# Optimization experiments

Measured on AMD Instinct MI355X. Metric: run time of the kernel, lower is better.

Reference implementation:

```python
import jax, jax.numpy as jnp
import numpy as np

B, S, D, H = 2, 2048, 1024, 16
DQ = D // H
EPS = 1e-5


def setup_inputs() -> dict:
    key = jax.random.key(0)
    ks = jax.random.split(key, 6)
    scale = 0.02
    return {
        "x": jax.random.normal(ks[0], (B, S, D), dtype=jnp.float32),
        "ln_g": jnp.ones((D,), dtype=jnp.float32),
        "ln_b": jnp.zeros((D,), dtype=jnp.float32),
        "Wq": jax.random.normal(ks[1], (D, D), dtype=jnp.float32) * scale,
        "bq": jnp.zeros((D,), dtype=jnp.float32),
        "Wk": jax.random.normal(ks[2], (D, D), dtype=jnp.float32) * scale,
        "bk": jnp.zeros((D,), dtype=jnp.float32),
        "Wv": jax.random.normal(ks[3], (D, D), dtype=jnp.float32) * scale,
        "bv": jnp.zeros((D,), dtype=jnp.float32),
        "Wo": jax.random.normal(ks[4], (D, D), dtype=jnp.float32) * scale,
        "bo": jnp.zeros((D,), dtype=jnp.float32),
    }


def reference(x, ln_g, ln_b, Wq, bq, Wk, bk, Wv, bv, Wo, bo):
    # pre-LayerNorm (torch default eps=1e-5, biased variance)
    mu = jnp.mean(x, axis=-1, keepdims=True)
    var = jnp.mean((x - mu) ** 2, axis=-1, keepdims=True)
    xn = (x - mu) * jax.lax.rsqrt(var + EPS) * ln_g + ln_b

    # QKV projections; weights stored [d_in, d_out]
    q = xn @ Wq + bq  # [B,S,D]
    k = xn @ Wk + bk
    v = xn @ Wv + bv

    # split heads -> [B,H,S,DQ]
    def heads(t):
        return t.reshape(B, S, H, DQ).transpose(0, 2, 1, 3)
    q, k, v = heads(q), heads(k), heads(v)

    scores = jnp.einsum("bhqd,bhkd->bhqk", q, k) / jnp.sqrt(jnp.float32(DQ))
    causal = jnp.tril(jnp.ones((S, S), dtype=bool))  # True = keep
    scores = jnp.where(causal, scores, -jnp.inf)
    probs = jax.nn.softmax(scores, axis=-1)
    attn = jnp.einsum("bhqk,bhkd->bhqd", probs, v)  # [B,H,S,DQ]

    # merge heads: [B,H,S,DQ] -> [B,S,H*DQ] (matches transpose/flatten/transpose)
    merged = attn.transpose(0, 2, 1, 3).reshape(B, S, D)
    out = merged @ Wo + bo
    return out + x
```

## Files before the change

### kernel.cpp

```cpp
#include <hip/hip_runtime.h>
#include <math.h>

#define BB 2
#define SS 2048
#define DD 1024
#define HH 16
#define DQK 64
#define NROWS (BB * SS)
#define NE ((size_t)BB * SS * DD)

using short8 = __attribute__((ext_vector_type(8))) short;
using f32x4  = __attribute__((ext_vector_type(4))) float;

__device__ __forceinline__ ushort f2bf(float f) {
  union { float f; unsigned u; } c; c.f = f;
  return (ushort)((c.u + 0x7fffu + ((c.u >> 16) & 1u)) >> 16);
}

__device__ __forceinline__ unsigned cvt_pk_bf16(float lo, float hi) {
  unsigned r;
  asm("v_cvt_pk_bf16_f32 %0, %1, %2" : "=v"(r) : "v"(lo), "v"(hi));
  return r;
}

__device__ __forceinline__ f32x4 mfma16(short8 a, short8 b, f32x4 c) {
  return __builtin_amdgcn_mfma_f32_16x16x32_bf16(a, b, c, 0, 0, 0);
}

typedef __attribute__((address_space(1))) const unsigned gas_u32;
typedef __attribute__((address_space(3))) unsigned las_u32;
__device__ __forceinline__ void gload_lds16(const void* g, void* l) {
  __builtin_amdgcn_global_load_lds((gas_u32*)g, (las_u32*)l, 16, 0, 0);
}

__global__ __launch_bounds__(256) void prep(const float* __restrict__ x,
                                            const float* __restrict__ g,
                                            const float* __restrict__ bta,
                                            ushort* __restrict__ xn,
                                            const float* __restrict__ Wq,
                                            const float* __restrict__ Wk,
                                            const float* __restrict__ Wv,
                                            const float* __restrict__ Wo,
                                            ushort* __restrict__ wt) {
  __shared__ float tile[64][65];
  const int t = threadIdx.x;
  if (blockIdx.x < NROWS) {
    const int row = blockIdx.x;
    float4 v = ((const float4*)(x + (size_t)row * DD))[t];
    float s  = v.x + v.y + v.z + v.w;
    float ss = v.x * v.x + v.y * v.y + v.z * v.z + v.w * v.w;
#pragma unroll
    for (int off = 32; off > 0; off >>= 1) {
      s  += __shfl_xor(s, off);
      ss += __shfl_xor(ss, off);
    }
    const int wid = t >> 6, lane = t & 63;
    if (lane == 0) { tile[0][wid] = s; tile[0][4 + wid] = ss; }
    __syncthreads();
    const float stot  = tile[0][0] + tile[0][1] + tile[0][2] + tile[0][3];
    const float sstot = tile[0][4] + tile[0][5] + tile[0][6] + tile[0][7];
    const float mu  = stot * (1.0f / DD);
    const float var = sstot * (1.0f / DD) - mu * mu;
    const float inv = rsqrtf(var + 1e-5f);
    const float4 g4 = ((const float4*)g)[t];
    const float4 b4 = ((const float4*)bta)[t];
    ushort4 o;
    o.x = f2bf((v.x - mu) * inv * g4.x + b4.x);
    o.y = f2bf((v.y - mu) * inv * g4.y + b4.y);
    o.z = f2bf((v.z - mu) * inv * g4.z + b4.z);
    o.w = f2bf((v.w - mu) * inv * g4.w + b4.w);
    ((ushort4*)(xn + (size_t)row * DD))[t] = o;
  } else {
    const int wb = blockIdx.x - NROWS;
    const int z = wb >> 8;
    const int k0 = (wb & 15) * 64, n0 = ((wb >> 4) & 15) * 64;
    const float* W = (z == 0) ? Wq : (z == 1) ? Wk : (z == 2) ? Wv : Wo;
    ushort* dst = wt + (size_t)z * DD * DD;
    const int tr = t >> 4, tc = (t & 15) * 4;
#pragma unroll
    for (int rr = 0; rr < 64; rr += 16) {
      float4 v = *(const float4*)(W + (size_t)(k0 + rr + tr) * DD + n0 + tc);
      tile[rr + tr][tc + 0] = v.x;
      tile[rr + tr][tc + 1] = v.y;
      tile[rr + tr][tc + 2] = v.z;
      tile[rr + tr][tc + 3] = v.w;
    }
    __syncthreads();
#pragma unroll
    for (int rr = 0; rr < 64; rr += 16) {
      const int n = rr + tr;
      ushort4 o;
      o.x = f2bf(tile[tc + 0][n]);
      o.y = f2bf(tile[tc + 1][n]);
      o.z = f2bf(tile[tc + 2][n]);
      o.w = f2bf(tile[tc + 3][n]);
      *(ushort4*)(dst + (size_t)(n0 + n) * DD + k0 + tc) = o;
    }
  }
}

#define GEMM_CORE(Ag, Bg)                                                     \
  f32x4 acc[4][4];                                                            \
  _Pragma("unroll")                                                           \
  for (int m = 0; m < 4; ++m)                                                 \
    _Pragma("unroll")                                                         \
    for (int n = 0; n < 4; ++n) acc[m][n] = (f32x4){0.f, 0.f, 0.f, 0.f};     \
  const int cs = ((t & 3) * 16) ^ (((t >> 2) & 3) * 16);                      \
  const int fsw = (r16 & 3) * 16;                                             \
  {                                                                           \
    GSTAGE(Ag, Bg, 0, 0);                                                     \
    int cur = 0;                                                              \
    for (int k0 = 0; k0 < DD; k0 += 32) {                                     \
      asm volatile("s_waitcnt vmcnt(0)" ::: "memory");                        \
      __syncthreads();                                                        \
      if (k0 + 32 < DD) GSTAGE(Ag, Bg, cur ^ 1, k0 + 32);                     \
      const char* Ac = (const char*)&As[cur][0][0];                           \
      const char* Bc = (const char*)&Bs[cur][0][0];                           \
      short8 af[4], bf[4];                                                    \
      _Pragma("unroll")                                                       \
      for (int m = 0; m < 4; ++m)                                             \
        af[m] = *(const short8*)(Ac + (wr * 64 + m * 16 + r16) * 64 +         \
                                 ((g * 16) ^ fsw));                           \
      _Pragma("unroll")                                                       \
      for (int n = 0; n < 4; ++n)                                             \
        bf[n] = *(const short8*)(Bc + (wc * 64 + n * 16 + r16) * 64 +         \
                                 ((g * 16) ^ fsw));                           \
      _Pragma("unroll")                                                       \
      for (int m = 0; m < 4; ++m)                                             \
        _Pragma("unroll")                                                     \
        for (int n = 0; n < 4; ++n) acc[m][n] = mfma16(af[m], bf[n], acc[m][n]); \
      cur ^= 1;                                                               \
    }                                                                         \
  }

#define GSTAGE(Ag, Bg, buf, k0)                                               \
  {                                                                           \
    _Pragma("unroll")                                                         \
    for (int i = 0; i < 2; ++i) {                                             \
      gload_lds16(Ag + (size_t)(row0 + i * 64 + (t >> 2)) * (DD * 2) +        \
                      (k0) * 2 + cs,                                          \
                  (char*)&As[buf][0][0] + i * 4096 + t * 16);                 \
      gload_lds16(Bg + (size_t)(col0 + i * 64 + (t >> 2)) * (DD * 2) +        \
                      (k0) * 2 + cs,                                          \
                  (char*)&Bs[buf][0][0] + i * 4096 + t * 16);                 \
    }                                                                         \
  }

__global__ __launch_bounds__(256) void gemm_qkv(
    const ushort* __restrict__ A, const ushort* __restrict__ wt,
    const float* __restrict__ bq, const float* __restrict__ bk,
    const float* __restrict__ bv, ushort* __restrict__ qb,
    ushort* __restrict__ kb, ushort* __restrict__ vt) {
  __shared__ ushort As[2][128][32];
  __shared__ ushort Bs[2][128][32];
  const int t = threadIdx.x;
  const int lane = t & 63;
  const int w = t >> 6, wr = w >> 1, wc = w & 1;
  const int r16 = lane & 15, g = lane >> 4;
  const int row0 = blockIdx.x * 128;
  const int mat = blockIdx.y >> 3;
  const int col0 = (blockIdx.y & 7) * 128;
  const char* Ag = (const char*)A;
  const char* Bg = (const char*)(wt + (size_t)mat * DD * DD);
  const float* bias = (mat == 0) ? bq : (mat == 1) ? bk : bv;
  const float scl = (mat == 0) ? 0.125f * 1.44269504f : 1.0f;

  GEMM_CORE(Ag, Bg)

#pragma unroll
  for (int n = 0; n < 4; ++n) {
    const int c = col0 + wc * 64 + n * 16 + r16;
    const float bc = bias[c];
#pragma unroll
    for (int m = 0; m < 4; ++m) {
      const int rbase = row0 + wr * 64 + m * 16 + g * 4;
      if (mat < 2) {
        ushort* outb = (mat == 0) ? qb : kb;
#pragma unroll
        for (int e = 0; e < 4; ++e)
          outb[(size_t)(rbase + e) * DD + c] = f2bf((acc[m][n][e] + bc) * scl);
      } else {
        uint2 st;
        st.x = cvt_pk_bf16(acc[m][n][0] + bc, acc[m][n][1] + bc);
        st.y = cvt_pk_bf16(acc[m][n][2] + bc, acc[m][n][3] + bc);
        const size_t vrow = (size_t)((rbase >> 11) * HH + (c >> 6)) * DQK + (c & 63);
        *(uint2*)(vt + vrow * SS + (rbase & 2047)) = st;
      }
    }
  }
}

__global__ __launch_bounds__(256) void gemm_o(
    const ushort* __restrict__ A, const ushort* __restrict__ Bt,
    const float* __restrict__ bias, const float* __restrict__ resid,
    float* __restrict__ outf) {
  __shared__ ushort As[2][128][32];
  __shared__ ushort Bs[2][128][32];
  const int t = threadIdx.x;
  const int lane = t & 63;
  const int w = t >> 6, wr = w >> 1, wc = w & 1;
  const int r16 = lane & 15, g = lane >> 4;
  const int row0 = blockIdx.x * 128;
  const int col0 = blockIdx.y * 128;
  const char* Ag = (const char*)A;
  const char* Bg = (const char*)Bt;

  GEMM_CORE(Ag, Bg)

#pragma unroll
  for (int n = 0; n < 4; ++n) {
    const int c = col0 + wc * 64 + n * 16 + r16;
    const float bc = bias[c];
#pragma unroll
    for (int m = 0; m < 4; ++m) {
      const int rbase = row0 + wr * 64 + m * 16 + g * 4;
#pragma unroll
      for (int e = 0; e < 4; ++e) {
        const size_t idx = (size_t)(rbase + e) * DD + c;
        outf[idx] = acc[m][n][e] + bc + resid[idx];
      }
    }
  }
}

__global__ __launch_bounds__(256) void attn_mfma(const ushort* __restrict__ Q,
                                                 const ushort* __restrict__ K,
                                                 const ushort* __restrict__ Vt,
                                                 ushort* __restrict__ O) {
  __shared__ ushort Ks[2][64][64];
  __shared__ ushort Vs[2][64][64];

  const int t = threadIdx.x, lane = t & 63, ww = t >> 6;
  const int r16 = lane & 15, g = lane >> 4;

  const int bid = blockIdx.x;
  const int xcd = bid & 7;
  const int bh = xcd * 4 + ((bid >> 3) & 3);
  const int m = (bid >> 5) & 7;
  const int j = bid >> 8;
  const int qb = (j == 0) ? (31 - m) : (j == 1) ? m : (j == 2) ? (23 - m) : (8 + m);
  const int b = bh >> 4, h = bh & 15;
  const size_t tokbase = (size_t)b * SS;
  const size_t hoff = (size_t)h * DQK;
  const int q0 = qb * 64 + ww * 16;
  const int nt = qb + 1;

  const int srow = t >> 3;
  const int scol = (t & 7) * 16;
  const char* Kb = (const char*)(K + tokbase * DD + hoff);
  const char* Vb = (const char*)(Vt + (size_t)bh * DQK * SS);
  const int sw = (r16 & 7) << 4;
  const int rlo = (r16 & 3) + ((r16 >> 2) << 3);

#define STAGE(buf, j0)                                                        \
  {                                                                           \
    _Pragma("unroll")                                                         \
    for (int i = 0; i < 2; ++i) {                                             \
      const int R = i * 32 + srow;                                            \
      const int Cs = scol ^ ((R & 7) << 4);                                   \
      gload_lds16(Kb + ((size_t)((j0) + R) * DD) * 2 + Cs,                    \
                  (char*)&Ks[buf][0][0] + i * 4096 + ww * 1024);              \
      gload_lds16(Vb + ((size_t)R * SS + (j0)) * 2 + Cs,                      \
                  (char*)&Vs[buf][0][0] + i * 4096 + ww * 1024);              \
    }                                                                         \
  }

  short8 qf[2];
#pragma unroll
  for (int kc = 0; kc < 2; ++kc)
    qf[kc] = *(const short8*)(Q + (tokbase + q0 + r16) * DD + hoff + kc * 32 + g * 8);

  f32x4 o[4];
#pragma unroll
  for (int dt = 0; dt < 4; ++dt) o[dt] = (f32x4){0.f, 0.f, 0.f, 0.f};
  float rm = -INFINITY, rl = 0.f;

  STAGE(0, 0);
  int cur = 0;
  for (int tt = 0; tt < nt; ++tt) {
    asm volatile("s_waitcnt vmcnt(0)" ::: "memory");
    __syncthreads();
    if (tt + 1 < nt) STAGE(cur ^ 1, (tt + 1) * 64);

    const char* Kc = (const char*)&Ks[cur][0][0];
    const char* Vc = (const char*)&Vs[cur][0][0];

    f32x4 s4[4];
    __builtin_amdgcn_s_setprio(1);
#pragma unroll
    for (int t2 = 0; t2 < 4; ++t2) {
      const int kk = rlo + (t2 & 1) * 4 + (t2 >> 1) * 32;
      const int sk = (kk & 7) << 4;
      const int rb = kk * 128;
      const short8 k0 = *(const short8*)(Kc + rb + ((g * 16) ^ sk));
      const short8 k1 = *(const short8*)(Kc + rb + ((64 + g * 16) ^ sk));
      f32x4 s = mfma16(k0, qf[0], (f32x4){0.f, 0.f, 0.f, 0.f});
      s4[t2] = mfma16(k1, qf[1], s);
    }
    __builtin_amdgcn_s_setprio(0);

    if (tt == nt - 1) {
      const int thrl = q0 + r16 - g * 8 - tt * 64;
#pragma unroll
      for (int t2 = 0; t2 < 4; ++t2) {
        const int bb = (t2 & 1) * 4 + (t2 >> 1) * 32;
#pragma unroll
        for (int r = 0; r < 4; ++r)
          s4[t2][r] = (bb + r <= thrl) ? s4[t2][r] : -INFINITY;
      }
    }

    float mx = fmaxf(
        fmaxf(fmaxf(fmaxf(s4[0][0], s4[0][1]), fmaxf(s4[0][2], s4[0][3])),
              fmaxf(fmaxf(s4[1][0], s4[1][1]), fmaxf(s4[1][2], s4[1][3]))),
        fmaxf(fmaxf(fmaxf(s4[2][0], s4[2][1]), fmaxf(s4[2][2], s4[2][3])),
              fmaxf(fmaxf(s4[3][0], s4[3][1]), fmaxf(s4[3][2], s4[3][3]))));

    if (!__all(mx - rm <= 8.f)) {
      float mf = fmaxf(mx, __shfl_xor(mx, 16));
      mf = fmaxf(mf, __shfl_xor(mf, 32));
      const float mn = fmaxf(rm, mf);
      const float sc = __builtin_amdgcn_exp2f(rm - mn);
      rl *= sc;
#pragma unroll
      for (int dt = 0; dt < 4; ++dt) o[dt] *= sc;
      rm = mn;
    }

    union { unsigned u[4]; short8 s; } pbu[2];
#pragma unroll
    for (int t2 = 0; t2 < 4; ++t2) {
      const float p0 = __builtin_amdgcn_exp2f(s4[t2][0] - rm);
      const float p1 = __builtin_amdgcn_exp2f(s4[t2][1] - rm);
      const float p2 = __builtin_amdgcn_exp2f(s4[t2][2] - rm);
      const float p3 = __builtin_amdgcn_exp2f(s4[t2][3] - rm);
      rl += (p0 + p1) + (p2 + p3);
      pbu[t2 >> 1].u[(t2 & 1) * 2 + 0] = cvt_pk_bf16(p0, p1);
      pbu[t2 >> 1].u[(t2 & 1) * 2 + 1] = cvt_pk_bf16(p2, p3);
    }

    __builtin_amdgcn_s_setprio(1);
#pragma unroll
    for (int kc = 0; kc < 2; ++kc) {
#pragma unroll
      for (int dt = 0; dt < 4; ++dt) {
        const short8 vf = *(const short8*)(Vc + (dt * 16 + r16) * 128 +
                                           ((kc * 64 + g * 16) ^ sw));
        o[dt] = mfma16(vf, pbu[kc].s, o[dt]);
      }
    }
    __builtin_amdgcn_s_setprio(0);
    cur ^= 1;
  }
#undef STAGE

  rl += __shfl_xor(rl, 16);
  rl += __shfl_xor(rl, 32);
  const float inv = 1.0f / rl;
#pragma unroll
  for (int dt = 0; dt < 4; ++dt) {
    uint2 st;
    st.x = cvt_pk_bf16(o[dt][0] * inv, o[dt][1] * inv);
    st.y = cvt_pk_bf16(o[dt][2] * inv, o[dt][3] * inv);
    *(uint2*)(O + (tokbase + q0 + r16) * DD + hoff + dt * 16 + g * 4) = st;
  }
}

extern "C" void kernel_launch(void* const* d_in, const int* in_sizes, int n_in,
                              void* d_out, int out_size, void* d_ws, size_t ws_size,
                              hipStream_t stream) {
  const float* x    = (const float*)d_in[0];
  const float* ln_g = (const float*)d_in[1];
  const float* ln_b = (const float*)d_in[2];
  const float* Wq   = (const float*)d_in[3];
  const float* bq   = (const float*)d_in[4];
  const float* Wk   = (const float*)d_in[5];
  const float* bk   = (const float*)d_in[6];
  const float* Wv   = (const float*)d_in[7];
  const float* bv   = (const float*)d_in[8];
  const float* Wo   = (const float*)d_in[9];
  const float* bo   = (const float*)d_in[10];
  float* out = (float*)d_out;

  ushort* ws  = (ushort*)d_ws;
  ushort* xn  = ws;
  ushort* qb  = xn + NE;
  ushort* kb  = qb + NE;
  ushort* vt  = kb + NE;
  ushort* ab  = vt + NE;
  ushort* wt  = ab + NE;
  ushort* wot = wt + (size_t)3 * DD * DD;

  prep<<<NROWS + 1024, 256, 0, stream>>>(x, ln_g, ln_b, xn, Wq, Wk, Wv, Wo, wt);

  gemm_qkv<<<dim3(NROWS / 128, 24), 256, 0, stream>>>(xn, wt, bq, bk, bv,
                                                      qb, kb, vt);

  attn_mfma<<<BB * HH * (SS / 64), 256, 0, stream>>>(qb, kb, vt, ab);

  gemm_o<<<dim3(NROWS / 128, DD / 128), 256, 0, stream>>>(ab, wot, bo, x, out);
}
```

Before: 115.0 us.

## Triple-buffer GEMM LDS staging and retune LDS swizzles in GEMM and attention

The GEMM main loop goes from double to triple buffering. It prefetches two k-steps ahead and waits with vmcnt(4) instead of draining all loads each iteration, to hide more global-load latency. The LDS XOR swizzle patterns in both the GEMM and attention kernels change, likely to reduce bank conflicts on ds_read. Plain __syncthreads is replaced by s_barrier wrapped in sched_barrier fences to control instruction scheduling. The cost is 50% more LDS per GEMM block, which could lower occupancy, and the vmcnt(4) count must match the number of loads GSTAGE issues.

```diff
diff --git a/kernel.cpp b/kernel.cpp
--- a/kernel.cpp
+++ b/kernel.cpp
@@ -105,17 +105,27 @@
   for (int m = 0; m < 4; ++m)                                                 \
     _Pragma("unroll")                                                         \
     for (int n = 0; n < 4; ++n) acc[m][n] = (f32x4){0.f, 0.f, 0.f, 0.f};     \
-  const int cs = ((t & 3) * 16) ^ (((t >> 2) & 3) * 16);                      \
-  const int fsw = (r16 & 3) * 16;                                             \
+  const int cs = ((t & 3) * 16) ^ (((t >> 3) & 3) * 16);                      \
+  const int fsw = ((r16 >> 1) & 3) * 16;                                      \
   {                                                                           \
     GSTAGE(Ag, Bg, 0, 0);                                                     \
-    int cur = 0;                                                              \
+    GSTAGE(Ag, Bg, 1, 32);                                                    \
+    int cb = 0;                                                               \
     for (int k0 = 0; k0 < DD; k0 += 32) {                                     \
-      asm volatile("s_waitcnt vmcnt(0)" ::: "memory");                        \
-      __syncthreads();                                                        \
-      if (k0 + 32 < DD) GSTAGE(Ag, Bg, cur ^ 1, k0 + 32);                     \
-      const char* Ac = (const char*)&As[cur][0][0];                           \
-      const char* Bc = (const char*)&Bs[cur][0][0];                           \
+      __builtin_amdgcn_sched_barrier(0);                                      \
+      if (k0 + 32 < DD) {                                                     \
+        asm volatile("s_waitcnt vmcnt(4)" ::: "memory");                      \
+      } else {                                                                \
+        asm volatile("s_waitcnt vmcnt(0)" ::: "memory");                      \
+      }                                                                       \
+      __builtin_amdgcn_s_barrier();                                           \
+      __builtin_amdgcn_sched_barrier(0);                                      \
+      if (k0 + 64 < DD) {                                                     \
+        int nb = cb + 2; if (nb >= 3) nb -= 3;                                \
+        GSTAGE(Ag, Bg, nb, k0 + 64);                                          \
+      }                                                                       \
+      const char* Ac = (const char*)&As[cb][0][0];                            \
+      const char* Bc = (const char*)&Bs[cb][0][0];                            \
       short8 af[4], bf[4];                                                    \
       _Pragma("unroll")                                                       \
       for (int m = 0; m < 4; ++m)                                             \
@@ -129,7 +139,7 @@
       for (int m = 0; m < 4; ++m)                                             \
         _Pragma("unroll")                                                     \
         for (int n = 0; n < 4; ++n) acc[m][n] = mfma16(af[m], bf[n], acc[m][n]); \
-      cur ^= 1;                                                               \
+      cb = (cb + 1 == 3) ? 0 : cb + 1;                                        \
     }                                                                         \
   }
 
@@ -151,8 +161,8 @@
     const float* __restrict__ bq, const float* __restrict__ bk,
     const float* __restrict__ bv, ushort* __restrict__ qb,
     ushort* __restrict__ kb, ushort* __restrict__ vt) {
-  __shared__ ushort As[2][128][32];
-  __shared__ ushort Bs[2][128][32];
+  __shared__ ushort As[3][128][32];
+  __shared__ ushort Bs[3][128][32];
   const int t = threadIdx.x;
   const int lane = t & 63;
   const int w = t >> 6, wr = w >> 1, wc = w & 1;
@@ -194,8 +204,8 @@
     const ushort* __restrict__ A, const ushort* __restrict__ Bt,
     const float* __restrict__ bias, const float* __restrict__ resid,
     float* __restrict__ outf) {
-  __shared__ ushort As[2][128][32];
-  __shared__ ushort Bs[2][128][32];
+  __shared__ ushort As[3][128][32];
+  __shared__ ushort Bs[3][128][32];
   const int t = threadIdx.x;
   const int lane = t & 63;
   const int w = t >> 6, wr = w >> 1, wc = w & 1;
@@ -249,7 +259,7 @@
   const int scol = (t & 7) * 16;
   const char* Kb = (const char*)(K + tokbase * DD + hoff);
   const char* Vb = (const char*)(Vt + (size_t)bh * DQK * SS);
-  const int sw = (r16 & 7) << 4;
+  const int sw = ((r16 & 3) | ((r16 >> 1) & 4)) << 4;
   const int rlo = (r16 & 3) + ((r16 >> 2) << 3);
 
 #define STAGE(buf, j0)                                                        \
@@ -257,7 +267,7 @@
     _Pragma("unroll")                                                         \
     for (int i = 0; i < 2; ++i) {                                             \
       const int R = i * 32 + srow;                                            \
-      const int Cs = scol ^ ((R & 7) << 4);                                   \
+      const int Cs = scol ^ (((R & 3) | ((R >> 1) & 4)) << 4);                \
       gload_lds16(Kb + ((size_t)((j0) + R) * DD) * 2 + Cs,                    \
                   (char*)&Ks[buf][0][0] + i * 4096 + ww * 1024);              \
       gload_lds16(Vb + ((size_t)R * SS + (j0)) * 2 + Cs,                      \
@@ -278,8 +288,10 @@
   STAGE(0, 0);
   int cur = 0;
   for (int tt = 0; tt < nt; ++tt) {
+    __builtin_amdgcn_sched_barrier(0);
     asm volatile("s_waitcnt vmcnt(0)" ::: "memory");
-    __syncthreads();
+    __builtin_amdgcn_s_barrier();
+    __builtin_amdgcn_sched_barrier(0);
     if (tt + 1 < nt) STAGE(cur ^ 1, (tt + 1) * 64);
 
     const char* Kc = (const char*)&Ks[cur][0][0];
@@ -290,7 +302,7 @@
 #pragma unroll
     for (int t2 = 0; t2 < 4; ++t2) {
       const int kk = rlo + (t2 & 1) * 4 + (t2 >> 1) * 32;
-      const int sk = (kk & 7) << 4;
+      const int sk = ((kk & 3) | ((kk >> 1) & 4)) << 4;
       const int rb = kk * 128;
       const short8 k0 = *(const short8*)(Kc + rb + ((g * 16) ^ sk));
       const short8 k1 = *(const short8*)(Kc + rb + ((64 + g * 16) ^ sk));
```

After: 107.8 us. -6.3%, faster.
